# Kernel optimization log

Hardware: AMD Instinct MI355X
Metric: run time of the kernel (lower is better)

Reference implementation:

```python
import jax, jax.numpy as jnp
import numpy as np

N_NODES = 100000
N_EDGES = 1000000
IN_CH = 64
OUT_CH = 16


def setup_inputs() -> dict:
    key = jax.random.key(0)
    ks = jax.random.split(key, 6)
    x = jax.random.normal(ks[0], (N_NODES, IN_CH), dtype=jnp.float32)
    W1 = jax.random.normal(ks[1], (IN_CH, IN_CH), dtype=jnp.float32) / np.sqrt(IN_CH)
    b1 = jax.random.normal(ks[2], (IN_CH,), dtype=jnp.float32) * 0.01
    W2 = jax.random.normal(ks[3], (IN_CH, OUT_CH), dtype=jnp.float32) / np.sqrt(IN_CH)
    b2 = jax.random.normal(ks[4], (OUT_CH,), dtype=jnp.float32) * 0.01
    edge_index = jax.random.randint(ks[5], (2, N_EDGES), 0, N_NODES, dtype=jnp.int64)
    return {"x": x, "W1": W1, "b1": b1, "W2": W2, "b2": b2,
            "edge_index": edge_index, "K": 3}


def _gcn_conv(x, W, b, src, dst, norm, n_nodes):
    # GCNConv: out = scatter_add(norm * (x @ W)[src], dst) + b
    h = x @ W                                   # [N, d_out]
    msg = h[src] * norm[:, None]                # [E+N, d_out] edge-wise gather
    agg = jax.ops.segment_sum(msg, dst, num_segments=n_nodes)
    return agg + b


def reference(x, W1, b1, W2, b2, edge_index, K):
    n = x.shape[0]
    loops = jnp.arange(n, dtype=edge_index.dtype)
    src = jnp.concatenate([edge_index[0], loops])  # A_hat = A + I
    dst = jnp.concatenate([edge_index[1], loops])
    # symmetric normalization deg^{-1/2} A_hat deg^{-1/2}
    deg = jnp.zeros((n,), dtype=x.dtype).at[dst].add(1.0)
    dinv = jax.lax.rsqrt(deg)  # deg >= 1 thanks to self-loops
    norm = dinv[src] * dinv[dst]
    for _ in range(K):
        x = _gcn_conv(x, W1, b1, src, dst, norm, n)
    return _gcn_conv(x, W2, b2, src, dst, norm, n)
```

## Files before the change

### kernel.cpp

```cpp
#include <hip/hip_runtime.h>
#include <hip/hip_bf16.h>
#include <stdint.h>

__device__ __forceinline__ float bf2f(unsigned short u) {
    unsigned int x = ((unsigned int)u) << 16;
    return __uint_as_float(x);
}
__device__ __forceinline__ unsigned short f2bf(float f) {
    unsigned int x = __float_as_uint(f);
    unsigned int lsb = (x >> 16) & 1u;
    x += 0x7fffu + lsb;
    return (unsigned short)(x >> 16);
}
__device__ __forceinline__ float loadF(const void* p, int i, int isbf) {
    return isbf ? bf2f(((const unsigned short*)p)[i]) : ((const float*)p)[i];
}

__global__ void k_init(const void* x, const void* eidx, int* flags, int* bcnt, int B) {
    int t = threadIdx.x;
    for (int b = t; b < B; b += blockDim.x) bcnt[b] = 0;
    if (t < 64) {
        const unsigned short* u = (const unsigned short*)x;
        float a = fabsf(bf2f(u[2 * t]));
        bool ok = (a == 0.0f) || (a > 1e-30f && a < 1e4f);
        unsigned long long mbf = __ballot(ok);
        if (t == 0) flags[0] = (mbf == ~0ULL) ? 1 : 0;
    } else if (t < 128) {
        int l = t - 64;
        const int* ip = (const int*)eidx;
        unsigned long long mi64 = __ballot(ip[2 * l + 1] == 0);
        if (l == 0) flags[1] = (mi64 == ~0ULL) ? 1 : 0;
    }
}

#define TS 68
__global__ void k_bin(const void* eidx, int E, int rsh, int B, int cap,
                      unsigned int* bins, int* bcnt, const int* flags,
                      const void* W1, const void* b1, const void* W2, const void* b2,
                      float* M, float* cvecs, int nbin) {
    if ((int)blockIdx.x == nbin) {
        __shared__ float A[64 * 64];
        __shared__ float T1[64 * TS];
        __shared__ float T2[64 * TS];
        __shared__ float B2s[64 * 16];
        __shared__ float bv[64], bw1[64], bw2[64];
        int bf = flags[0];
        int t = threadIdx.x;
        if (t < 256) {
            for (int i = t; i < 4096; i += 256) A[i] = loadF(W1, i, bf);
            for (int i = t; i < 1024; i += 256) B2s[i] = loadF(W2, i, bf);
            if (t < 64) bv[t] = loadF(b1, t, bf);
        }
        __syncthreads();
        if (t < 256) {
            const int i0 = (t >> 4) * 4;
            const int j0 = (t & 15) * 4;
            {
                float acc[4][4] = {};
#pragma unroll 8
                for (int k = 0; k < 64; ++k) {
                    float a0 = A[(i0 + 0) * 64 + k];
                    float a1 = A[(i0 + 1) * 64 + k];
                    float a2 = A[(i0 + 2) * 64 + k];
                    float a3 = A[(i0 + 3) * 64 + k];
                    float4 bq = *(const float4*)&A[k * 64 + j0];
                    acc[0][0] += a0 * bq.x; acc[0][1] += a0 * bq.y; acc[0][2] += a0 * bq.z; acc[0][3] += a0 * bq.w;
                    acc[1][0] += a1 * bq.x; acc[1][1] += a1 * bq.y; acc[1][2] += a1 * bq.z; acc[1][3] += a1 * bq.w;
                    acc[2][0] += a2 * bq.x; acc[2][1] += a2 * bq.y; acc[2][2] += a2 * bq.z; acc[2][3] += a2 * bq.w;
                    acc[3][0] += a3 * bq.x; acc[3][1] += a3 * bq.y; acc[3][2] += a3 * bq.z; acc[3][3] += a3 * bq.w;
                }
#pragma unroll
                for (int ii = 0; ii < 4; ++ii)
                    *(float4*)&T1[(i0 + ii) * TS + j0] = make_float4(acc[ii][0], acc[ii][1], acc[ii][2], acc[ii][3]);
            }
            if (t < 64) {
                float acc = 0.f;
#pragma unroll 8
                for (int i = 0; i < 64; ++i) acc += bv[i] * A[i * 64 + t];
                bw1[t] = acc;
            }
        }
        __syncthreads();
        if (t < 256) {
            const int i0 = (t >> 4) * 4;
            const int j0 = (t & 15) * 4;
            {
                float acc[4][4] = {};
#pragma unroll 8
                for (int k = 0; k < 64; ++k) {
                    float a0 = T1[(i0 + 0) * TS + k];
                    float a1 = T1[(i0 + 1) * TS + k];
                    float a2 = T1[(i0 + 2) * TS + k];
                    float a3 = T1[(i0 + 3) * TS + k];
                    float4 bq = *(const float4*)&A[k * 64 + j0];
                    acc[0][0] += a0 * bq.x; acc[0][1] += a0 * bq.y; acc[0][2] += a0 * bq.z; acc[0][3] += a0 * bq.w;
                    acc[1][0] += a1 * bq.x; acc[1][1] += a1 * bq.y; acc[1][2] += a1 * bq.z; acc[1][3] += a1 * bq.w;
                    acc[2][0] += a2 * bq.x; acc[2][1] += a2 * bq.y; acc[2][2] += a2 * bq.z; acc[2][3] += a2 * bq.w;
                    acc[3][0] += a3 * bq.x; acc[3][1] += a3 * bq.y; acc[3][2] += a3 * bq.z; acc[3][3] += a3 * bq.w;
                }
#pragma unroll
                for (int ii = 0; ii < 4; ++ii)
                    *(float4*)&T2[(i0 + ii) * TS + j0] = make_float4(acc[ii][0], acc[ii][1], acc[ii][2], acc[ii][3]);
            }
            if (t < 64) {
                float acc = 0.f;
#pragma unroll 8
                for (int i = 0; i < 64; ++i) acc += bw1[i] * A[i * 64 + t];
                bw2[t] = acc;
            }
        }
        __syncthreads();
        if (t < 256) {
            {
                int i = t >> 2, j0m = (t & 3) * 4;
                float4 acc = {0.f, 0.f, 0.f, 0.f};
#pragma unroll 8
                for (int k = 0; k < 64; ++k) {
                    float a = T2[i * TS + k];
                    float4 bq = *(const float4*)&B2s[k * 16 + j0m];
                    acc.x += a * bq.x; acc.y += a * bq.y; acc.z += a * bq.z; acc.w += a * bq.w;
                }
                *(float4*)&M[i * 16 + j0m] = acc;
            }
            if (t < 16) {
                float a3 = 0.f, a2 = 0.f, a1 = 0.f;
#pragma unroll 8
                for (int i = 0; i < 64; ++i) {
                    float w = B2s[i * 16 + t];
                    a3 += bw2[i] * w;
                    a2 += bw1[i] * w;
                    a1 += bv[i] * w;
                }
                cvecs[t] = a3;
                cvecs[16 + t] = a2;
                cvecs[32 + t] = a1;
                cvecs[48 + t] = loadF(b2, t, flags[0]);
            }
        }
        return;
    }
    extern __shared__ int sh[];
    int* hist   = sh;
    int* base_s = sh + B;
    const int i64 = flags[1];
    const int t = threadIdx.x, nt = blockDim.x;
    const long long i0 = (long long)blockIdx.x * E / nbin;
    const long long i1 = (long long)(blockIdx.x + 1) * E / nbin;
    const long long* e64 = (const long long*)eidx;
    const int* e32 = (const int*)eidx;
    const int mask = (1 << rsh) - 1;

    for (int b = t; b < B; b += nt) hist[b] = 0;
    __syncthreads();
    for (long long i = i0 + t; i < i1; i += nt) {
        int d = i64 ? (int)e64[E + i] : e32[E + i];
        atomicAdd(&hist[d >> rsh], 1);
    }
    __syncthreads();
    for (int b = t; b < B; b += nt) {
        int c = hist[b];
        base_s[b] = c ? atomicAdd(&bcnt[b], c) : 0;
        hist[b] = 0;
    }
    __syncthreads();
    for (long long i = i0 + t; i < i1; i += nt) {
        int d, s;
        if (i64) { d = (int)e64[E + i]; s = (int)e64[i]; }
        else     { d = e32[E + i];     s = e32[i]; }
        int b = d >> rsh;
        int pos = base_s[b] + atomicAdd(&hist[b], 1);
        if (pos >= cap) pos = cap - 1;
        bins[(size_t)b * cap + pos] = ((unsigned int)s << rsh) | (unsigned int)(d & mask);
    }
}

__global__ void k_csr(const unsigned int* bins, const int* bcnt, int cap, int rsh,
                      int n, int* colb, int4* meta) {
    __shared__ int dh[128], db[128], ch[128];
    const int R = 1 << rsh;
    const int b = blockIdx.x, t = threadIdx.x, nt = blockDim.x;
    const int mask = R - 1;
    for (int r = t; r < R; r += nt) { dh[r] = 0; ch[r] = 0; }
    __syncthreads();
    int cnt = bcnt[b]; if (cnt > cap) cnt = cap;
    const unsigned int* eb = bins + (size_t)b * cap;
    for (int e = t; e < cnt; e += nt)
        atomicAdd(&dh[eb[e] & mask], 1);
    __syncthreads();
    if (t < R) db[t] = dh[t];
    __syncthreads();
    for (int off = 1; off < R; off <<= 1) {
        int add = 0;
        if (t < R && t >= off) add = db[t - off];
        __syncthreads();
        if (t < R) db[t] += add;
        __syncthreads();
    }
    const int v0 = b << rsh;
    const int gbase = b * cap;
    if (t < R) {
        int v = v0 + t;
        if (v < n) {
            int len = dh[t];
            float dv = rsqrtf((float)(len + 1));
            meta[v] = make_int4(gbase + db[t] - len, len, __float_as_int(dv), 0);
        }
    }
    __syncthreads();
    for (int e = t; e < cnt; e += nt) {
        unsigned int w = eb[e];
        int r = w & mask;
        int pos = (db[r] - dh[r]) + atomicAdd(&ch[r], 1);
        colb[gbase + pos] = (int)(w >> rsh);
    }
}

__global__ void k_xm(const void* x, const float* M, const int4* meta,
                     unsigned short* z0, int n, const int* flags) {
    __shared__ float Ms[64 * 16];
    __shared__ float xs[16 * 64];
    int bf = flags[0];
    int t = threadIdx.x;
    ((float4*)Ms)[t] = ((const float4*)M)[t];
    int base = blockIdx.x * 16;
    if (!bf) {
        int row = base + (t >> 4);
        float4 v = make_float4(0.f, 0.f, 0.f, 0.f);
        if (row < n) v = ((const float4*)x)[base * 16 + t];
        ((float4*)xs)[t] = v;
    } else {
        for (int k = t; k < 1024; k += 256) {
            int r = k >> 6, cc = k & 63;
            int row = base + r;
            xs[k] = (row < n) ? bf2f(((const unsigned short*)x)[row * 64 + cc]) : 0.f;
        }
    }
    __syncthreads();
    int r = t >> 4, c = t & 15;
    int row = base + r;
    if (row < n) {
        float acc = 0.f;
#pragma unroll
        for (int k = 0; k < 64; ++k) acc += xs[r * 64 + k] * Ms[k * 16 + c];
        float dv = __int_as_float(meta[row].z);
        z0[row * 16 + c] = f2bf(dv * acc);
    }
}

__global__ void k_prop(const unsigned short* zin, void* yout, const int4* meta,
                       const int* colb, const float* cvec,
                       int n, int is_final, const int* flags) {
    int tid = blockIdx.x * blockDim.x + threadIdx.x;
    int v = tid >> 2, q = tid & 3;
    if (v >= n) return;
    int4 m = meta[v];
    int beg = m.x, len = m.y;
    ushort4 sv = *(const ushort4*)&zin[(size_t)v * 16 + q * 4];
    float4 acc = make_float4(bf2f(sv.x), bf2f(sv.y), bf2f(sv.z), bf2f(sv.w));
    int j = beg, end = beg + len;
    for (; j + 4 <= end; j += 4) {
        int c0 = colb[j], c1 = colb[j + 1], c2 = colb[j + 2], c3 = colb[j + 3];
        ushort4 za = *(const ushort4*)&zin[(size_t)c0 * 16 + q * 4];
        ushort4 zb = *(const ushort4*)&zin[(size_t)c1 * 16 + q * 4];
        ushort4 zc = *(const ushort4*)&zin[(size_t)c2 * 16 + q * 4];
        ushort4 zd = *(const ushort4*)&zin[(size_t)c3 * 16 + q * 4];
        acc.x += (bf2f(za.x) + bf2f(zb.x)) + (bf2f(zc.x) + bf2f(zd.x));
        acc.y += (bf2f(za.y) + bf2f(zb.y)) + (bf2f(zc.y) + bf2f(zd.y));
        acc.z += (bf2f(za.z) + bf2f(zb.z)) + (bf2f(zc.z) + bf2f(zd.z));
        acc.w += (bf2f(za.w) + bf2f(zb.w)) + (bf2f(zc.w) + bf2f(zd.w));
    }
    for (; j < end; ++j) {
        int c0 = colb[j];
        ushort4 za = *(const ushort4*)&zin[(size_t)c0 * 16 + q * 4];
        acc.x += bf2f(za.x); acc.y += bf2f(za.y); acc.z += bf2f(za.z); acc.w += bf2f(za.w);
    }
    float dv = __int_as_float(m.z);
    float a = is_final ? dv : dv * dv;
    float b = is_final ? 1.0f : dv;
    float4 cv = *(const float4*)&cvec[q * 4];
    float4 val;
    val.x = a * acc.x + b * cv.x;
    val.y = a * acc.y + b * cv.y;
    val.z = a * acc.z + b * cv.z;
    val.w = a * acc.w + b * cv.w;
    int o = v * 16 + q * 4;
    if (is_final) {
        if (flags[0]) {
            ushort4 ov;
            ov.x = f2bf(val.x); ov.y = f2bf(val.y); ov.z = f2bf(val.z); ov.w = f2bf(val.w);
            *(ushort4*)&((unsigned short*)yout)[o] = ov;
        } else {
            *(float4*)&((float*)yout)[o] = val;
        }
    } else {
        ushort4 ov;
        ov.x = f2bf(val.x); ov.y = f2bf(val.y); ov.z = f2bf(val.z); ov.w = f2bf(val.w);
        *(ushort4*)&((unsigned short*)yout)[o] = ov;
    }
}

extern "C" void kernel_launch(void* const* d_in, const int* in_sizes, int n_in,
                              void* d_out, int out_size, void* d_ws, size_t ws_size,
                              hipStream_t stream) {
    const void* x  = d_in[0];
    const void* W1 = d_in[1];
    const void* b1 = d_in[2];
    const void* W2 = d_in[3];
    const void* b2 = d_in[4];
    const void* ei = d_in[5];

    const int n = in_sizes[0] / 64;
    const int E = in_sizes[5] / 2;

    const int rsh = 7;
    const int B = (n + (1 << rsh) - 1) >> rsh;
    const int avg = E / B;
    int cap = avg + avg / 4 + 128;
    cap = (cap + 31) & ~31;

    char* base = (char*)d_ws;
    size_t off = 0;
    auto carve = [&](size_t bytes) -> void* {
        void* r = base + off;
        off = (off + bytes + 255) & ~(size_t)255;
        return r;
    };
    int*            flags  = (int*)carve(8);
    int*            bcnt   = (int*)carve((size_t)B * 4);
    unsigned int*   bins   = (unsigned int*)carve((size_t)B * cap * 4);
    int*            colb   = (int*)carve((size_t)B * cap * 4);
    int4*           meta   = (int4*)carve((size_t)n * 16);
    float*          Mm     = (float*)carve(1024 * 4);
    float*          cvecs  = (float*)carve(64 * 4);
    unsigned short* z0     = (unsigned short*)carve((size_t)n * 16 * 2);
    unsigned short* z1     = (unsigned short*)carve((size_t)n * 16 * 2);
    (void)ws_size; (void)n_in; (void)out_size;

    const int nbin = 240;
    k_init<<<1, 1024, 0, stream>>>(x, ei, flags, bcnt, B);
    k_bin<<<nbin + 1, 512, (size_t)2 * B * 4, stream>>>(ei, E, rsh, B, cap, bins, bcnt,
                                                        flags, W1, b1, W2, b2, Mm, cvecs, nbin);
    k_csr<<<B, 256, 0, stream>>>(bins, bcnt, cap, rsh, n, colb, meta);
    k_xm<<<(n + 15) / 16, 256, 0, stream>>>(x, Mm, meta, z0, n, flags);

    const int pgrid = (n * 4 + 255) / 256;
    k_prop<<<pgrid, 256, 0, stream>>>(z0, z1, meta, colb, cvecs + 0,  n, 0, flags);
    k_prop<<<pgrid, 256, 0, stream>>>(z1, z0, meta, colb, cvecs + 16, n, 0, flags);
    k_prop<<<pgrid, 256, 0, stream>>>(z0, z1, meta, colb, cvecs + 32, n, 0, flags);
    k_prop<<<pgrid, 256, 0, stream>>>(z1, d_out, meta, colb, cvecs + 48, n, 1, flags);
}
```

Before: 100.5 us.

## Pad CSR rows to multiples of four and use two threads per node

Each node's neighbour list is padded to a multiple of four entries. The padding points at an extra zero row appended to each feature buffer, so the propagation loop can read column indices as int4 with no scalar tail loop. Propagation now uses 2 threads per node with 16-byte int4 gathers (8 bf16 each) instead of 4 threads with 8-byte loads, which halves the thread count and doubles the bytes per load. In exchange it does extra gathers on padded zero entries, uses more registers per thread, and relies on the added per-row padding fitting within the enlarged capP bucket size.

```diff
diff --git a/kernel.cpp b/kernel.cpp
--- a/kernel.cpp
+++ b/kernel.cpp
@@ -12,13 +12,21 @@
     x += 0x7fffu + lsb;
     return (unsigned short)(x >> 16);
 }
+__device__ __forceinline__ unsigned int pack2bf(float lo, float hi) {
+    return (unsigned int)f2bf(lo) | ((unsigned int)f2bf(hi) << 16);
+}
+__device__ __forceinline__ float bflo(unsigned int u) { return __uint_as_float(u << 16); }
+__device__ __forceinline__ float bfhi(unsigned int u) { return __uint_as_float(u & 0xffff0000u); }
 __device__ __forceinline__ float loadF(const void* p, int i, int isbf) {
     return isbf ? bf2f(((const unsigned short*)p)[i]) : ((const float*)p)[i];
 }
 
-__global__ void k_init(const void* x, const void* eidx, int* flags, int* bcnt, int B) {
+__global__ void k_init(const void* x, const void* eidx, int* flags, int* bcnt, int B,
+                       unsigned int* z0s, unsigned int* z1s) {
     int t = threadIdx.x;
     for (int b = t; b < B; b += blockDim.x) bcnt[b] = 0;
+    if (t < 8) z0s[t] = 0;
+    else if (t < 16) z1s[t - 8] = 0;
     if (t < 64) {
         const unsigned short* u = (const unsigned short*)x;
         float a = fabsf(bf2f(u[2 * t]));
@@ -174,9 +182,9 @@
     }
 }
 
-__global__ void k_csr(const unsigned int* bins, const int* bcnt, int cap, int rsh,
-                      int n, int* colb, int4* meta) {
-    __shared__ int dh[128], db[128], ch[128];
+__global__ void k_csr(const unsigned int* bins, const int* bcnt, int cap, int capP,
+                      int rsh, int n, int* colb, int4* meta) {
+    __shared__ int dh[128], db[128], pl[128], ch[128];
     const int R = 1 << rsh;
     const int b = blockIdx.x, t = threadIdx.x, nt = blockDim.x;
     const int mask = R - 1;
@@ -187,7 +195,7 @@
     for (int e = t; e < cnt; e += nt)
         atomicAdd(&dh[eb[e] & mask], 1);
     __syncthreads();
-    if (t < R) db[t] = dh[t];
+    if (t < R) { pl[t] = (dh[t] + 3) & ~3; db[t] = pl[t]; }
     __syncthreads();
     for (int off = 1; off < R; off <<= 1) {
         int add = 0;
@@ -197,20 +205,22 @@
         __syncthreads();
     }
     const int v0 = b << rsh;
-    const int gbase = b * cap;
+    const int gbase = b * capP;
     if (t < R) {
         int v = v0 + t;
         if (v < n) {
             int len = dh[t];
             float dv = rsqrtf((float)(len + 1));
-            meta[v] = make_int4(gbase + db[t] - len, len, __float_as_int(dv), 0);
+            int rs = gbase + db[t] - pl[t];
+            meta[v] = make_int4(rs, len, __float_as_int(dv), 0);
+            for (int p = len; p < pl[t]; ++p) colb[rs + p] = n;
         }
     }
     __syncthreads();
     for (int e = t; e < cnt; e += nt) {
         unsigned int w = eb[e];
         int r = w & mask;
-        int pos = (db[r] - dh[r]) + atomicAdd(&ch[r], 1);
+        int pos = (db[r] - pl[r]) + atomicAdd(&ch[r], 1);
         colb[gbase + pos] = (int)(w >> rsh);
     }
 }
@@ -251,51 +261,64 @@
                        const int* colb, const float* cvec,
                        int n, int is_final, const int* flags) {
     int tid = blockIdx.x * blockDim.x + threadIdx.x;
-    int v = tid >> 2, q = tid & 3;
+    int v = tid >> 1, h = tid & 1;
     if (v >= n) return;
     int4 m = meta[v];
     int beg = m.x, len = m.y;
-    ushort4 sv = *(const ushort4*)&zin[(size_t)v * 16 + q * 4];
-    float4 acc = make_float4(bf2f(sv.x), bf2f(sv.y), bf2f(sv.z), bf2f(sv.w));
-    int j = beg, end = beg + len;
-    for (; j + 4 <= end; j += 4) {
-        int c0 = colb[j], c1 = colb[j + 1], c2 = colb[j + 2], c3 = colb[j + 3];
-        ushort4 za = *(const ushort4*)&zin[(size_t)c0 * 16 + q * 4];
-        ushort4 zb = *(const ushort4*)&zin[(size_t)c1 * 16 + q * 4];
-        ushort4 zc = *(const ushort4*)&zin[(size_t)c2 * 16 + q * 4];
-        ushort4 zd = *(const ushort4*)&zin[(size_t)c3 * 16 + q * 4];
-        acc.x += (bf2f(za.x) + bf2f(zb.x)) + (bf2f(zc.x) + bf2f(zd.x));
-        acc.y += (bf2f(za.y) + bf2f(zb.y)) + (bf2f(zc.y) + bf2f(zd.y));
-        acc.z += (bf2f(za.z) + bf2f(zb.z)) + (bf2f(zc.z) + bf2f(zd.z));
-        acc.w += (bf2f(za.w) + bf2f(zb.w)) + (bf2f(zc.w) + bf2f(zd.w));
-    }
-    for (; j < end; ++j) {
-        int c0 = colb[j];
-        ushort4 za = *(const ushort4*)&zin[(size_t)c0 * 16 + q * 4];
-        acc.x += bf2f(za.x); acc.y += bf2f(za.y); acc.z += bf2f(za.z); acc.w += bf2f(za.w);
+    int padlen = (len + 3) & ~3;
+    int4 sw = *(const int4*)&zin[(size_t)v * 16 + h * 8];
+    float a0 = bflo((unsigned)sw.x), a1 = bfhi((unsigned)sw.x);
+    float a2 = bflo((unsigned)sw.y), a3 = bfhi((unsigned)sw.y);
+    float a4 = bflo((unsigned)sw.z), a5 = bfhi((unsigned)sw.z);
+    float a6 = bflo((unsigned)sw.w), a7 = bfhi((unsigned)sw.w);
+    for (int j = beg; j < beg + padlen; j += 4) {
+        int4 cc = *(const int4*)&colb[j];
+        int4 za = *(const int4*)&zin[(size_t)cc.x * 16 + h * 8];
+        int4 zb = *(const int4*)&zin[(size_t)cc.y * 16 + h * 8];
+        int4 zc = *(const int4*)&zin[(size_t)cc.z * 16 + h * 8];
+        int4 zd = *(const int4*)&zin[(size_t)cc.w * 16 + h * 8];
+        a0 += (bflo((unsigned)za.x) + bflo((unsigned)zb.x)) + (bflo((unsigned)zc.x) + bflo((unsigned)zd.x));
+        a1 += (bfhi((unsigned)za.x) + bfhi((unsigned)zb.x)) + (bfhi((unsigned)zc.x) + bfhi((unsigned)zd.x));
+        a2 += (bflo((unsigned)za.y) + bflo((unsigned)zb.y)) + (bflo((unsigned)zc.y) + bflo((unsigned)zd.y));
+        a3 += (bfhi((unsigned)za.y) + bfhi((unsigned)zb.y)) + (bfhi((unsigned)zc.y) + bfhi((unsigned)zd.y));
+        a4 += (bflo((unsigned)za.z) + bflo((unsigned)zb.z)) + (bflo((unsigned)zc.z) + bflo((unsigned)zd.z));
+        a5 += (bfhi((unsigned)za.z) + bfhi((unsigned)zb.z)) + (bfhi((unsigned)zc.z) + bfhi((unsigned)zd.z));
+        a6 += (bflo((unsigned)za.w) + bflo((unsigned)zb.w)) + (bflo((unsigned)zc.w) + bflo((unsigned)zd.w));
+        a7 += (bfhi((unsigned)za.w) + bfhi((unsigned)zb.w)) + (bfhi((unsigned)zc.w) + bfhi((unsigned)zd.w));
     }
     float dv = __int_as_float(m.z);
-    float a = is_final ? dv : dv * dv;
-    float b = is_final ? 1.0f : dv;
-    float4 cv = *(const float4*)&cvec[q * 4];
-    float4 val;
-    val.x = a * acc.x + b * cv.x;
-    val.y = a * acc.y + b * cv.y;
-    val.z = a * acc.z + b * cv.z;
-    val.w = a * acc.w + b * cv.w;
-    int o = v * 16 + q * 4;
+    float sa = is_final ? dv : dv * dv;
+    float sb = is_final ? 1.0f : dv;
+    float4 cv0 = *(const float4*)&cvec[h * 8];
+    float4 cv1 = *(const float4*)&cvec[h * 8 + 4];
+    float r0 = sa * a0 + sb * cv0.x;
+    float r1 = sa * a1 + sb * cv0.y;
+    float r2 = sa * a2 + sb * cv0.z;
+    float r3 = sa * a3 + sb * cv0.w;
+    float r4 = sa * a4 + sb * cv1.x;
+    float r5 = sa * a5 + sb * cv1.y;
+    float r6 = sa * a6 + sb * cv1.z;
+    float r7 = sa * a7 + sb * cv1.w;
     if (is_final) {
         if (flags[0]) {
-            ushort4 ov;
-            ov.x = f2bf(val.x); ov.y = f2bf(val.y); ov.z = f2bf(val.z); ov.w = f2bf(val.w);
-            *(ushort4*)&((unsigned short*)yout)[o] = ov;
+            int4 ov;
+            ov.x = (int)pack2bf(r0, r1);
+            ov.y = (int)pack2bf(r2, r3);
+            ov.z = (int)pack2bf(r4, r5);
+            ov.w = (int)pack2bf(r6, r7);
+            *(int4*)&((unsigned short*)yout)[(size_t)v * 16 + h * 8] = ov;
         } else {
-            *(float4*)&((float*)yout)[o] = val;
+            float* o = &((float*)yout)[(size_t)v * 16 + h * 8];
+            *(float4*)o = make_float4(r0, r1, r2, r3);
+            *(float4*)(o + 4) = make_float4(r4, r5, r6, r7);
         }
     } else {
-        ushort4 ov;
-        ov.x = f2bf(val.x); ov.y = f2bf(val.y); ov.z = f2bf(val.z); ov.w = f2bf(val.w);
-        *(ushort4*)&((unsigned short*)yout)[o] = ov;
+        int4 ov;
+        ov.x = (int)pack2bf(r0, r1);
+        ov.y = (int)pack2bf(r2, r3);
+        ov.z = (int)pack2bf(r4, r5);
+        ov.w = (int)pack2bf(r6, r7);
+        *(int4*)&((unsigned short*)yout)[(size_t)v * 16 + h * 8] = ov;
     }
 }
 
@@ -317,6 +340,7 @@
     const int avg = E / B;
     int cap = avg + avg / 4 + 128;
     cap = (cap + 31) & ~31;
+    const int capP = cap + 512;
 
     char* base = (char*)d_ws;
     size_t off = 0;
@@ -328,22 +352,24 @@
     int*            flags  = (int*)carve(8);
     int*            bcnt   = (int*)carve((size_t)B * 4);
     unsigned int*   bins   = (unsigned int*)carve((size_t)B * cap * 4);
-    int*            colb   = (int*)carve((size_t)B * cap * 4);
+    int*            colb   = (int*)carve((size_t)B * capP * 4);
     int4*           meta   = (int4*)carve((size_t)n * 16);
     float*          Mm     = (float*)carve(1024 * 4);
     float*          cvecs  = (float*)carve(64 * 4);
-    unsigned short* z0     = (unsigned short*)carve((size_t)n * 16 * 2);
-    unsigned short* z1     = (unsigned short*)carve((size_t)n * 16 * 2);
+    unsigned short* z0     = (unsigned short*)carve(((size_t)n + 1) * 16 * 2);
+    unsigned short* z1     = (unsigned short*)carve(((size_t)n + 1) * 16 * 2);
     (void)ws_size; (void)n_in; (void)out_size;
 
     const int nbin = 240;
-    k_init<<<1, 1024, 0, stream>>>(x, ei, flags, bcnt, B);
+    k_init<<<1, 1024, 0, stream>>>(x, ei, flags, bcnt, B,
+                                   (unsigned int*)&z0[(size_t)n * 16],
+                                   (unsigned int*)&z1[(size_t)n * 16]);
     k_bin<<<nbin + 1, 512, (size_t)2 * B * 4, stream>>>(ei, E, rsh, B, cap, bins, bcnt,
                                                         flags, W1, b1, W2, b2, Mm, cvecs, nbin);
-    k_csr<<<B, 256, 0, stream>>>(bins, bcnt, cap, rsh, n, colb, meta);
+    k_csr<<<B, 256, 0, stream>>>(bins, bcnt, cap, capP, rsh, n, colb, meta);
     k_xm<<<(n + 15) / 16, 256, 0, stream>>>(x, Mm, meta, z0, n, flags);
 
-    const int pgrid = (n * 4 + 255) / 256;
+    const int pgrid = (n * 2 + 255) / 256;
     k_prop<<<pgrid, 256, 0, stream>>>(z0, z1, meta, colb, cvecs + 0,  n, 0, flags);
     k_prop<<<pgrid, 256, 0, stream>>>(z1, z0, meta, colb, cvecs + 16, n, 0, flags);
     k_prop<<<pgrid, 256, 0, stream>>>(z0, z1, meta, colb, cvecs + 32, n, 0, flags);
```

After: 102.1 us. No clear change (+1.6%).
